# Performance work log

Hardware: AMD Instinct MI355X
Metric: run time of the kernel (lower is better)

## Reference

```python
import jax, jax.numpy as jnp
import numpy as np

GRID_SIZE = 20
GRID_MIN, GRID_MAX = -2.0, 2.0
SIGMA = (GRID_MAX - GRID_MIN) / (GRID_SIZE - 1)  # RBF width = grid spacing


def setup_inputs() -> dict:
    key = jax.random.key(0)
    k1, k2, k3 = jax.random.split(key, 3)
    batch, in_features, out_features = 4096, 1024, 1024
    x = jax.random.normal(k1, (batch, in_features), dtype=jnp.float32)
    # glorot-scale initializations for faithfulness to keras glorot_uniform magnitude
    lim_b = np.sqrt(6.0 / (in_features + out_features))
    base_weight = jax.random.uniform(k2, (in_features, out_features), jnp.float32, -lim_b, lim_b)
    lim_s = np.sqrt(6.0 / (in_features * GRID_SIZE + out_features))
    spline_weight = jax.random.uniform(k3, (in_features, GRID_SIZE, out_features), jnp.float32, -lim_s, lim_s)
    mu = jnp.linspace(GRID_MIN, GRID_MAX, GRID_SIZE, dtype=jnp.float32)
    return {"x": x, "base_weight": base_weight, "spline_weight": spline_weight, "mu": mu}


def reference(x, base_weight, spline_weight, mu):
    # base path: SiLU(x) @ W_base
    base_out = jnp.einsum('bi,io->bo', jax.nn.silu(x), base_weight)
    # RBF basis expansion: [b, i, g]
    diff = (x[..., None] - mu) / SIGMA
    basis = jnp.exp(-(diff * diff))
    spline_out = jnp.einsum('big,igo->bo', basis, spline_weight)
    return base_out + spline_out
```

## Files before the change

### kernel.cpp

```cpp
#include <hip/hip_runtime.h>
#include <hip/hip_bf16.h>
#include <stdint.h>


typedef short short8 __attribute__((ext_vector_type(8)));
typedef __bf16 bf16x8 __attribute__((ext_vector_type(8)));
typedef float f32x4 __attribute__((ext_vector_type(4)));
typedef unsigned int u32;

__device__ __forceinline__ unsigned short f2bf(float f) {
  __hip_bfloat16 h = __float2bfloat16(f);
  return __builtin_bit_cast(unsigned short, h);
}

__device__ __forceinline__ void gload_lds16(const unsigned short* g, unsigned short* l) {
  __builtin_amdgcn_global_load_lds(
      (const __attribute__((address_space(1))) u32*)(const void*)g,
      (__attribute__((address_space(3))) u32*)(void*)l, 16, 0, 0);
}


__global__ void prep_silu(const float* __restrict__ x, unsigned short* __restrict__ A, int ld) {
  int g = blockIdx.x * 256 + threadIdx.x;
  int row = g >> 7;
  int col = (g & 127) * 8;
  const float4* x4 = reinterpret_cast<const float4*>(x);
  float4 a = x4[g * 2], b = x4[g * 2 + 1];
  float v[8] = {a.x, a.y, a.z, a.w, b.x, b.y, b.z, b.w};
  union { unsigned short u[8]; short8 v8; } o;
#pragma unroll
  for (int j = 0; j < 8; ++j) {
    float s = v[j] / (1.f + __expf(-v[j]));
    o.u[j] = f2bf(s);
  }
  *reinterpret_cast<short8*>(&A[(size_t)row * ld + col]) = o.v8;
}

__global__ void prep_basis(const float* __restrict__ x, unsigned short* __restrict__ A,
                           int i0, int L, int ld, int col_off) {
  int g = blockIdx.x * 256 + threadIdx.x;
  int e0 = g * 8;
  int b = e0 / L;
  int k0 = e0 - b * L;
  const float* xr = x + (size_t)b * 1024 + i0;
  union { unsigned short u[8]; short8 v8; } o;
#pragma unroll
  for (int j = 0; j < 8; ++j) {
    int k = k0 + j;
    int il = (int)(((unsigned)k * 104858u) >> 21);
    int gg = k - il * 20;
    float xv = xr[il];
    float d = (xv + 2.0f) * 4.75f - (float)gg;
    o.u[j] = f2bf(__expf(-d * d));
  }
  *reinterpret_cast<short8*>(&A[(size_t)b * ld + col_off + k0]) = o.v8;
}

__global__ void prep_wt(const float* __restrict__ W, unsigned short* __restrict__ Bt,
                        int Kp, int ldbt, int k_off) {
  __shared__ unsigned short tile[64][72];
  int tiles_k = Kp >> 6;
  int bk = blockIdx.x % tiles_k, bn = blockIdx.x / tiles_k;
  int t = threadIdx.x;
  int lr = t >> 4;
  int lc = (t & 15) * 4;
#pragma unroll
  for (int r = 0; r < 4; ++r) {
    int row = r * 16 + lr;
    float4 v = *reinterpret_cast<const float4*>(&W[(size_t)(bk * 64 + row) * 1024 + bn * 64 + lc]);
    tile[row][lc + 0] = f2bf(v.x);
    tile[row][lc + 1] = f2bf(v.y);
    tile[row][lc + 2] = f2bf(v.z);
    tile[row][lc + 3] = f2bf(v.w);
  }
  __syncthreads();
  int nr = t >> 3;
  int kc = (t & 7) * 8;
#pragma unroll
  for (int r = 0; r < 2; ++r) {
    int n = r * 32 + nr;
    union { unsigned short u[8]; short8 v8; } o;
#pragma unroll
    for (int j = 0; j < 8; ++j) o.u[j] = tile[kc + j][n];
    *reinterpret_cast<short8*>(&Bt[(size_t)(bn * 64 + n) * ldbt + k_off + bk * 64 + kc]) = o.v8;
  }
}

__global__ __launch_bounds__(256, 4) void gemm_bf16(
    const unsigned short* __restrict__ A, int lda,
    const unsigned short* __restrict__ Bt, int ldb,
    float* __restrict__ C, int Kz) {
  const int tid = threadIdx.x;
  const int wid = tid >> 6, lane = tid & 63;

  const int cpx = gridDim.x >> 3;
  const int wg = (blockIdx.x & 7) * cpx + (blockIdx.x >> 3);
  const int mtile = wg & 31;
  const int ntile = (wg >> 5) & 7;
  const int z = wg >> 8;
  const int brow = mtile * 128, bcol = ntile * 128;
  const int kbase = z * Kz;

  __shared__ __align__(16) unsigned short As[128 * 64];
  __shared__ __align__(16) unsigned short Bs[128 * 64];

  const int srow = wid * 32 + (lane >> 3);
  const int scol = ((lane & 7) ^ (lane >> 3)) * 8;
  const unsigned short* aptr = A + (size_t)(brow + srow) * lda + kbase + scol;
  const unsigned short* bptr = Bt + (size_t)(bcol + srow) * ldb + kbase + scol;
  unsigned short* lA = &As[wid * 2048];
  unsigned short* lB = &Bs[wid * 2048];

  const int wr = wid >> 1, wc = wid & 1;
  const int fr = lane & 15;
  const int fg = lane >> 4;

  f32x4 acc[4][4] = {};

  for (int kt = 0; kt < Kz; kt += 64) {
#pragma unroll
    for (int c = 0; c < 4; ++c)
      gload_lds16(aptr + (size_t)(c * 8) * lda, lA + c * 512);
#pragma unroll
    for (int c = 0; c < 4; ++c)
      gload_lds16(bptr + (size_t)(c * 8) * ldb, lB + c * 512);
    aptr += 64;
    bptr += 64;
    __syncthreads();
#pragma unroll
    for (int ks = 0; ks < 2; ++ks) {
      bf16x8 af[4], bfr[4];
#pragma unroll
      for (int m = 0; m < 4; ++m) {
        int row = wr * 64 + m * 16 + fr;
        int cp = ((ks * 4 + fg) ^ (fr & 7)) * 8;
        af[m] = __builtin_bit_cast(
            bf16x8, *reinterpret_cast<const short8*>(&As[row * 64 + cp]));
      }
#pragma unroll
      for (int n = 0; n < 4; ++n) {
        int row = wc * 64 + n * 16 + fr;
        int cp = ((ks * 4 + fg) ^ (fr & 7)) * 8;
        bfr[n] = __builtin_bit_cast(
            bf16x8, *reinterpret_cast<const short8*>(&Bs[row * 64 + cp]));
      }
#pragma unroll
      for (int m = 0; m < 4; ++m)
#pragma unroll
        for (int n = 0; n < 4; ++n)
          acc[m][n] = __builtin_amdgcn_mfma_f32_16x16x32_bf16(af[m], bfr[n], acc[m][n], 0, 0, 0);
    }
    __syncthreads();
  }

  const int r0 = brow + wr * 64 + (lane >> 4) * 4;
  const int c0 = bcol + wc * 64 + (lane & 15);
#pragma unroll
  for (int m = 0; m < 4; ++m)
#pragma unroll
    for (int n = 0; n < 4; ++n)
#pragma unroll
      for (int j = 0; j < 4; ++j) {
        size_t idx = (size_t)(r0 + m * 16 + j) * 1024 + (c0 + n * 16);
        atomicAdd(&C[idx], acc[m][n][j]);
      }
}


extern "C" void kernel_launch(void* const* d_in, const int* in_sizes, int n_in,
                              void* d_out, int out_size, void* d_ws, size_t ws_size,
                              hipStream_t stream) {
  (void)in_sizes; (void)n_in; (void)out_size;
  const float* x = (const float*)d_in[0];
  const float* Wb = (const float*)d_in[1];
  const float* Ws = (const float*)d_in[2];
  float* out = (float*)d_out;
  char* ws = (char*)d_ws;

  int npass = 16;
  for (int np = 2; np <= 16; np <<= 1) {
    size_t K0 = 1024 + (1024 / np) * 20;
    size_t need = 4096ull * K0 * 2 + 1024ull * K0 * 2;
    if (need <= ws_size) { npass = np; break; }
  }
  const int CI = 1024 / npass;
  const int K0 = 1024 + CI * 20;
  const int Ksp = CI * 20;
  unsigned short* A2  = (unsigned short*)ws;
  unsigned short* W2t = (unsigned short*)(ws + 4096ull * K0 * 2);

  hipMemsetAsync(out, 0, 4096ull * 1024 * 4, stream);

  for (int p = 0; p < npass; ++p) {
    const int Kfull = (p == 0) ? K0 : Ksp;
    const int col_off = (p == 0) ? 1024 : 0;
    if (p == 0) {
      prep_silu<<<2048, 256, 0, stream>>>(x, A2, Kfull);
      prep_wt<<<256, 256, 0, stream>>>(Wb, W2t, 1024, Kfull, 0);
    }
    prep_basis<<<4096 * Ksp / 8 / 256, 256, 0, stream>>>(x, A2, p * CI, Ksp, Kfull, col_off);
    prep_wt<<<(Ksp / 64) * 16, 256, 0, stream>>>(Ws + (size_t)p * Ksp * 1024, W2t, Ksp, Kfull, col_off);
    gemm_bf16<<<1024, 256, 0, stream>>>(A2, Kfull, W2t, Kfull, out, Kfull / 4);
  }
}
```

Before: 436.8 us.

## Use 256x256 tiles with double-buffered async LDS pipeline in GEMM

Replaces the 128x128 single-buffered GEMM with a 256x256 tile, 512-thread kernel that double-buffers global-to-LDS loads, prefetching two K-tiles ahead with explicit vmcnt waits and raising wave priority during the MFMA phase. Larger tiles raise arithmetic intensity and cut the number of split-K atomic adds. Overlapping loads with compute is meant to hide global memory latency. The cost is 128KB of LDS per block and many more accumulators per thread, which lowers occupancy, and the grid shrinks to 256 blocks, which may underfill the GPU's compute units.

Result: no change. 438.0 us (+0.3%).

```diff
diff --git a/kernel.cpp b/kernel.cpp
--- a/kernel.cpp
+++ b/kernel.cpp
@@ -7,6 +7,10 @@
 typedef __bf16 bf16x8 __attribute__((ext_vector_type(8)));
 typedef float f32x4 __attribute__((ext_vector_type(4)));
 typedef unsigned int u32;
+
+#define VMCNT8() asm volatile("s_waitcnt vmcnt(8)" ::: "memory")
+#define VMCNT0() asm volatile("s_waitcnt vmcnt(0)" ::: "memory")
+#define LGKM0()  asm volatile("s_waitcnt lgkmcnt(0)" ::: "memory")
 
 __device__ __forceinline__ unsigned short f2bf(float f) {
   __hip_bfloat16 h = __float2bfloat16(f);
@@ -86,77 +90,93 @@
   }
 }
 
-__global__ __launch_bounds__(256, 4) void gemm_bf16(
+__global__ __launch_bounds__(512, 2) void gemm256(
     const unsigned short* __restrict__ A, int lda,
     const unsigned short* __restrict__ Bt, int ldb,
     float* __restrict__ C, int Kz) {
+  __shared__ __align__(16) unsigned short lds[2][2][256 * 64];
+
   const int tid = threadIdx.x;
   const int wid = tid >> 6, lane = tid & 63;
 
   const int cpx = gridDim.x >> 3;
-  const int wg = (blockIdx.x & 7) * cpx + (blockIdx.x >> 3);
-  const int mtile = wg & 31;
-  const int ntile = (wg >> 5) & 7;
-  const int z = wg >> 8;
-  const int brow = mtile * 128, bcol = ntile * 128;
+  const int wg = ((int)blockIdx.x & 7) * cpx + ((int)blockIdx.x >> 3);
+  const int mtile = wg & 15;
+  const int ntile = (wg >> 4) & 3;
+  const int z = wg >> 6;
+  const int brow = mtile * 256, bcol = ntile * 256;
   const int kbase = z * Kz;
-
-  __shared__ __align__(16) unsigned short As[128 * 64];
-  __shared__ __align__(16) unsigned short Bs[128 * 64];
-
-  const int srow = wid * 32 + (lane >> 3);
+  const int NT = Kz >> 6;
+
+  const int srow = wid * 8 + (lane >> 3);
   const int scol = ((lane & 7) ^ (lane >> 3)) * 8;
-  const unsigned short* aptr = A + (size_t)(brow + srow) * lda + kbase + scol;
-  const unsigned short* bptr = Bt + (size_t)(bcol + srow) * ldb + kbase + scol;
-  unsigned short* lA = &As[wid * 2048];
-  unsigned short* lB = &Bs[wid * 2048];
-
-  const int wr = wid >> 1, wc = wid & 1;
-  const int fr = lane & 15;
-  const int fg = lane >> 4;
-
-  f32x4 acc[4][4] = {};
-
-  for (int kt = 0; kt < Kz; kt += 64) {
-#pragma unroll
-    for (int c = 0; c < 4; ++c)
-      gload_lds16(aptr + (size_t)(c * 8) * lda, lA + c * 512);
-#pragma unroll
-    for (int c = 0; c < 4; ++c)
-      gload_lds16(bptr + (size_t)(c * 8) * ldb, lB + c * 512);
-    aptr += 64;
-    bptr += 64;
-    __syncthreads();
-#pragma unroll
-    for (int ks = 0; ks < 2; ++ks) {
-      bf16x8 af[4], bfr[4];
-#pragma unroll
-      for (int m = 0; m < 4; ++m) {
-        int row = wr * 64 + m * 16 + fr;
-        int cp = ((ks * 4 + fg) ^ (fr & 7)) * 8;
-        af[m] = __builtin_bit_cast(
-            bf16x8, *reinterpret_cast<const short8*>(&As[row * 64 + cp]));
+  const unsigned short* aS = A + (size_t)(brow + srow) * lda + kbase + scol;
+  const unsigned short* bS = Bt + (size_t)(bcol + srow) * ldb + kbase + scol;
+  const int lOff = wid * 512;
+
+  const int wm = wid >> 2, wn = wid & 3;
+  const int fr = lane & 15, fg = lane >> 4;
+  const int cp0 = ((fg) ^ (fr & 7)) * 8;
+  const int cp1 = ((4 + fg) ^ (fr & 7)) * 8;
+
+  f32x4 acc[8][4] = {};
+
+#define STAGE(t_, buf_)                                                        \
+  {                                                                            \
+    const unsigned short* a_ = aS + (t_) * 64;                                 \
+    const unsigned short* b_ = bS + (t_) * 64;                                 \
+    _Pragma("unroll") for (int cc = 0; cc < 4; ++cc) {                         \
+      gload_lds16(a_ + (size_t)(cc * 64) * lda, &lds[buf_][0][lOff + cc * 4096]); \
+      gload_lds16(b_ + (size_t)(cc * 64) * ldb, &lds[buf_][1][lOff + cc * 4096]); \
+    }                                                                          \
+  }
+
+  STAGE(0, 0);
+  STAGE(1, 1);
+
+  for (int t = 0; t < NT; ++t) {
+    const int c = t & 1;
+    if (t == NT - 1) { VMCNT0(); } else { VMCNT8(); }
+    __builtin_amdgcn_s_barrier();
+
+    bf16x8 af[8][2], bfr[4][2];
+#pragma unroll
+    for (int m = 0; m < 8; ++m) {
+      int row = wm * 128 + m * 16 + fr;
+      af[m][0] = __builtin_bit_cast(bf16x8,
+          *reinterpret_cast<const short8*>(&lds[c][0][row * 64 + cp0]));
+      af[m][1] = __builtin_bit_cast(bf16x8,
+          *reinterpret_cast<const short8*>(&lds[c][0][row * 64 + cp1]));
+    }
+#pragma unroll
+    for (int n = 0; n < 4; ++n) {
+      int row = wn * 64 + n * 16 + fr;
+      bfr[n][0] = __builtin_bit_cast(bf16x8,
+          *reinterpret_cast<const short8*>(&lds[c][1][row * 64 + cp0]));
+      bfr[n][1] = __builtin_bit_cast(bf16x8,
+          *reinterpret_cast<const short8*>(&lds[c][1][row * 64 + cp1]));
+    }
+    LGKM0();
+    __builtin_amdgcn_s_barrier();
+
+    if (t + 2 < NT) STAGE(t + 2, c);
+
+    __builtin_amdgcn_s_setprio(1);
+#pragma unroll
+    for (int m = 0; m < 8; ++m)
+#pragma unroll
+      for (int n = 0; n < 4; ++n) {
+        f32x4 tmp = __builtin_amdgcn_mfma_f32_16x16x32_bf16(af[m][0], bfr[n][0], acc[m][n], 0, 0, 0);
+        acc[m][n] = __builtin_amdgcn_mfma_f32_16x16x32_bf16(af[m][1], bfr[n][1], tmp, 0, 0, 0);
       }
-#pragma unroll
-      for (int n = 0; n < 4; ++n) {
-        int row = wc * 64 + n * 16 + fr;
-        int cp = ((ks * 4 + fg) ^ (fr & 7)) * 8;
-        bfr[n] = __builtin_bit_cast(
-            bf16x8, *reinterpret_cast<const short8*>(&Bs[row * 64 + cp]));
-      }
-#pragma unroll
-      for (int m = 0; m < 4; ++m)
-#pragma unroll
-        for (int n = 0; n < 4; ++n)
-          acc[m][n] = __builtin_amdgcn_mfma_f32_16x16x32_bf16(af[m], bfr[n], acc[m][n], 0, 0, 0);
-    }
-    __syncthreads();
-  }
-
-  const int r0 = brow + wr * 64 + (lane >> 4) * 4;
-  const int c0 = bcol + wc * 64 + (lane & 15);
-#pragma unroll
-  for (int m = 0; m < 4; ++m)
+    __builtin_amdgcn_s_setprio(0);
+  }
+#undef STAGE
+
+  const int r0 = brow + wm * 128 + (lane >> 4) * 4;
+  const int c0 = bcol + wn * 64 + (lane & 15);
+#pragma unroll
+  for (int m = 0; m < 8; ++m)
 #pragma unroll
     for (int n = 0; n < 4; ++n)
 #pragma unroll
@@ -200,6 +220,6 @@
     }
     prep_basis<<<4096 * Ksp / 8 / 256, 256, 0, stream>>>(x, A2, p * CI, Ksp, Kfull, col_off);
     prep_wt<<<(Ksp / 64) * 16, 256, 0, stream>>>(Ws + (size_t)p * Ksp * 1024, W2t, Ksp, Kfull, col_off);
-    gemm_bf16<<<1024, 256, 0, stream>>>(A2, Kfull, W2t, Kfull, out, Kfull / 4);
-  }
-}
+    gemm256<<<256, 512, 0, stream>>>(A2, Kfull, W2t, Kfull, out, Kfull / 4);
+  }
+}
```
